# Kernel tuning notes

Measured on AMD Instinct MI355X. Metric: run time of the kernel, lower is better.

Reference implementation:

```python
import jax, jax.numpy as jnp
import numpy as np

N = 100_000; E = 1_600_000; G = 64
D_IN = 128; POS = 16; HID = 32; HEADS = 4; OUT = 10
D0 = D_IN + POS; D1 = HID * HEADS
LRELU = 0.2; BN_EPS = 1e-5; DIV_W = 0.1


def setup_inputs() -> dict:
    key = jax.random.key(0)
    k = jax.random.split(key, 24)
    nrm = lambda ki, shape, s: jax.random.normal(ki, shape, dtype=jnp.float32) * s
    inp = {}
    inp["x"] = nrm(k[0], (N, D_IN), 1.0)
    inp["edge_index"] = jax.random.randint(k[1], (2, E), 0, N, dtype=jnp.int32)
    inp["batch"] = jnp.sort(jax.random.randint(k[2], (N,), 0, G, dtype=jnp.int32))
    inp["pos_w"] = nrm(k[3], (2, POS), 0.5)
    inp["pos_b"] = nrm(k[4], (POS,), 0.1)
    inp["w0"] = nrm(k[5], (D0, HEADS * HID), D0 ** -0.5)
    inp["asrc0"] = nrm(k[6], (HEADS, HID), HID ** -0.5)
    inp["adst0"] = nrm(k[7], (HEADS, HID), HID ** -0.5)
    inp["b0"] = nrm(k[8], (D1,), 0.1)
    inp["w1"] = nrm(k[9], (D1, HEADS * HID), D1 ** -0.5)
    inp["asrc1"] = nrm(k[10], (HEADS, HID), HID ** -0.5)
    inp["adst1"] = nrm(k[11], (HEADS, HID), HID ** -0.5)
    inp["b1"] = nrm(k[12], (D1,), 0.1)
    inp["bn_gamma"] = 1.0 + nrm(k[13], (2, D1), 0.1)
    inp["bn_beta"] = nrm(k[14], (2, D1), 0.1)
    inp["bn_mean"] = nrm(k[15], (2, D1), 0.1)
    inp["bn_var"] = jax.random.uniform(k[16], (2, D1), dtype=jnp.float32, minval=0.5, maxval=1.5)
    inp["proj"] = nrm(k[17], (2, HEADS, HID), HID ** -0.5)
    inp["res_w"] = nrm(k[18], (D1, D1), D1 ** -0.5)
    inp["res_b"] = nrm(k[19], (D1,), 0.1)
    inp["task_w"] = nrm(k[20], (D1, OUT), D1 ** -0.5)
    inp["task_b"] = nrm(k[21], (OUT,), 0.1)
    return inp


def _positions(batch):
    # vectorized version of the per-node Python loop: grid layout per graph
    counts = jnp.bincount(batch, length=G)               # nodes per graph
    starts = jnp.cumsum(counts) - counts                  # exclusive cumsum
    local = jnp.arange(N, dtype=counts.dtype) - starts[batch]
    grid = jnp.ceil(jnp.sqrt(counts.astype(jnp.float32))).astype(counts.dtype)
    g = jnp.maximum(grid[batch], 1)
    denom = jnp.maximum(g - 1, 1).astype(jnp.float32)
    row = (local // g).astype(jnp.float32)
    col = (local % g).astype(jnp.float32)
    return jnp.stack([row / denom, col / denom], axis=-1)  # (N, 2)


def _gat(x, src, dst, w, a_src, a_dst, bias):
    # PyG GATConv (v1) with self-loops already appended to src/dst
    n = x.shape[0]
    h = (x @ w).reshape(n, HEADS, HID)                     # (N, H, C)
    e = jax.nn.leaky_relu(jnp.sum(h * a_src, -1)[src] + jnp.sum(h * a_dst, -1)[dst], LRELU)  # (E+N, H)
    m = jax.lax.stop_gradient(jax.ops.segment_max(e, dst, num_segments=n))
    ex = jnp.exp(e - m[dst])
    alpha = ex / jax.ops.segment_sum(ex, dst, num_segments=n)[dst]
    out = jax.ops.segment_sum(alpha[:, :, None] * h[src], dst, num_segments=n)
    return out.reshape(n, D1) + bias


def _div_loss(x, proj):
    # per-head projection, then mean pairwise cosine similarity between heads
    p = x.reshape(-1, HEADS, HID) * proj                   # (N, H, C)
    pn = p / jnp.maximum(jnp.linalg.norm(p, axis=-1, keepdims=True), 1e-8)
    M = jnp.einsum('nhd,ngd->hg', pn, pn) / pn.shape[0]    # mean_n cos(h_i, h_j)
    iu = jnp.triu_indices(HEADS, k=1)
    return jnp.mean(M[iu] ** 2)


def _bn(x, gamma, beta, mean, var):
    return (x - mean) * gamma * jax.lax.rsqrt(var + BN_EPS) + beta


def reference(x, edge_index, batch, pos_w, pos_b, w0, asrc0, adst0, b0,
              w1, asrc1, adst1, b1, bn_gamma, bn_beta, bn_mean, bn_var,
              proj, res_w, res_b, task_w, task_b):
    loops = jnp.arange(N, dtype=edge_index.dtype)
    src = jnp.concatenate([edge_index[0], loops])
    dst = jnp.concatenate([edge_index[1], loops])
    pos = _positions(batch)
    h = jnp.concatenate([x, pos @ pos_w + pos_b], axis=1)  # (N, D0)
    # layer 0
    h = _gat(h, src, dst, w0, asrc0, adst0, b0)
    div = _div_loss(h, proj[0])
    h = jax.nn.elu(_bn(h, bn_gamma[0], bn_beta[0], bn_mean[0], bn_var[0]))
    # layer 1 (+ residual projection of previous activation)
    prev = h
    h = _gat(h, src, dst, w1, asrc1, adst1, b1)
    div = div + _div_loss(h, proj[1])
    h = jax.nn.elu(_bn(h, bn_gamma[1], bn_beta[1], bn_mean[1], bn_var[1]))
    h = h + prev @ res_w + res_b
    # global mean pool over graphs
    counts = jnp.bincount(batch, length=G).astype(h.dtype)
    emb = jax.ops.segment_sum(h, batch, num_segments=G) / jnp.maximum(counts, 1.0)[:, None]
    task = emb @ task_w + task_b
    return task, DIV_W * div, emb
```

## Files before the change

### kernel.cpp

```cpp
#include <hip/hip_runtime.h>
#include <hip/hip_bf16.h>

#define N_NODES 100000
#define N_EDGES 1600000
#define G_GRAPHS 64
#define D_IN 128
#define POS_DIM 16
#define HID 32
#define HEADS 4
#define OUT_DIM 10
#define D0 144
#define D1 128
#define LRELU_SLOPE 0.2f
#define BN_EPS 1e-5f
#define DIV_W 0.1f

#define BK_SHIFT 9
#define BK_NODES 512
#define NB 196
#define TILE_E 4096
#define NTILES ((N_EDGES + TILE_E - 1) / TILE_E)

#define K0P 160
#define AGG_BLOCKS 2048
#define AGG_WAVES (AGG_BLOCKS * 4)

typedef __attribute__((ext_vector_type(8))) short short8v;
typedef __attribute__((ext_vector_type(4))) float f32x4;

__device__ __forceinline__ unsigned short f2b(float f) {
    unsigned u = __float_as_uint(f);
    unsigned r = (u + 0x7FFFu + ((u >> 16) & 1u)) >> 16;
    return (unsigned short)r;
}
__device__ __forceinline__ float blo(unsigned v) { return __uint_as_float(v << 16); }
__device__ __forceinline__ float bhi(unsigned v) { return __uint_as_float(v & 0xFFFF0000u); }

__global__ void k_hist(const int* __restrict__ batch, int* __restrict__ counts, int n) {
    __shared__ int hist[G_GRAPHS];
    if (threadIdx.x < G_GRAPHS) hist[threadIdx.x] = 0;
    __syncthreads();
    for (int i = blockIdx.x * blockDim.x + threadIdx.x; i < n; i += gridDim.x * blockDim.x)
        atomicAdd(&hist[batch[i]], 1);
    __syncthreads();
    if (threadIdx.x < G_GRAPHS) atomicAdd(&counts[threadIdx.x], hist[threadIdx.x]);
}

__global__ void k_gridstats(const int* __restrict__ counts, int* __restrict__ starts,
                            int* __restrict__ gridg) {
    if (threadIdx.x == 0) {
        int run = 0;
        for (int g = 0; g < G_GRAPHS; ++g) {
            starts[g] = run;
            int c = counts[g];
            run += c;
            int s = (int)sqrtf((float)c);
            while ((long long)s * s < c) ++s;
            while (s > 0 && (long long)(s - 1) * (s - 1) >= c) --s;
            gridg[g] = s;
        }
    }
}

__global__ void k_pos(const int* __restrict__ batch, const int* __restrict__ starts,
                      const int* __restrict__ gridg, float2* __restrict__ pos2) {
    int t = blockIdx.x * blockDim.x + threadIdx.x;
    if (t >= N_NODES) return;
    int b = batch[t];
    int local = t - starts[b];
    int g = max(gridg[b], 1);
    float denom = (float)max(g - 1, 1);
    int r = local / g;
    int c = local - r * g;
    pos2[t] = make_float2((float)r / denom, (float)c / denom);
}

__global__ void k_wprep(const float* __restrict__ w0, const float* __restrict__ w1,
                        const float* __restrict__ wr, unsigned short* __restrict__ t0,
                        unsigned short* __restrict__ t1, unsigned short* __restrict__ tr) {
    int t = blockIdx.x * 256 + threadIdx.x;
    if (t < 128 * K0P) {
        int c = t / K0P, k = t % K0P;
        t0[t] = (k < D0) ? f2b(w0[k * 128 + c]) : (unsigned short)0;
    } else if (t < 128 * K0P + 128 * 128) {
        int i = t - 128 * K0P;
        int c = i / 128, k = i % 128;
        t1[i] = f2b(w1[k * 128 + c]);
    } else if (t < 128 * K0P + 2 * 128 * 128) {
        int i = t - 128 * K0P - 128 * 128;
        int c = i / 128, k = i % 128;
        tr[i] = f2b(wr[k * 128 + c]);
    }
}

__global__ void k_bhist(const int* __restrict__ ei, int* __restrict__ bcount) {
    __shared__ int lh[256];
    int tid = threadIdx.x;
    lh[tid] = 0;
    __syncthreads();
    int e = (blockIdx.x * blockDim.x + tid) * 4;
    if (e < N_EDGES) {
        int4 d4 = *reinterpret_cast<const int4*>(ei + N_EDGES + e);
        atomicAdd(&lh[d4.x >> BK_SHIFT], 1);
        atomicAdd(&lh[d4.y >> BK_SHIFT], 1);
        atomicAdd(&lh[d4.z >> BK_SHIFT], 1);
        atomicAdd(&lh[d4.w >> BK_SHIFT], 1);
    }
    __syncthreads();
    if (tid < NB && lh[tid] > 0) atomicAdd(&bcount[tid], lh[tid]);
}

__global__ void k_bscan(const int* __restrict__ bcount, int* __restrict__ bstart,
                        int* __restrict__ bcursor) {
    if (threadIdx.x == 0) {
        int run = 0;
        for (int i = 0; i < NB; ++i) {
            bstart[i] = run;
            bcursor[i] = run;
            run += bcount[i];
        }
        bstart[NB] = run;
    }
}

__global__ __launch_bounds__(256) void k_bucket(const int* __restrict__ ei,
                                                int* __restrict__ bcursor,
                                                int2* __restrict__ pairs) {
    __shared__ int lh[256];
    __shared__ int lstart[256];
    __shared__ int lcur[256];
    __shared__ int gbase[256];
    __shared__ int2 stage[TILE_E];
    const int tid = threadIdx.x;
    const int tile = blockIdx.x * TILE_E;
    const int cnt = min(TILE_E, N_EDGES - tile);
    lh[tid] = 0;
    __syncthreads();
    int sv[16], dv[16];
#pragma unroll
    for (int u = 0; u < 16; ++u) {
        int i = u * 256 + tid;
        if (i < cnt) {
            sv[u] = ei[tile + i];
            dv[u] = ei[N_EDGES + tile + i];
            atomicAdd(&lh[dv[u] >> BK_SHIFT], 1);
        } else {
            sv[u] = -1; dv[u] = -1;
        }
    }
    __syncthreads();
    int own = lh[tid];
    lstart[tid] = own;
    __syncthreads();
    for (int off = 1; off < 256; off <<= 1) {
        int add = (tid >= off) ? lstart[tid - off] : 0;
        __syncthreads();
        lstart[tid] += add;
        __syncthreads();
    }
    int excl = lstart[tid] - own;
    __syncthreads();
    lstart[tid] = excl;
    lcur[tid] = excl;
    __syncthreads();
#pragma unroll
    for (int u = 0; u < 16; ++u) {
        if (dv[u] >= 0) {
            int b = dv[u] >> BK_SHIFT;
            int slot = atomicAdd(&lcur[b], 1);
            stage[slot] = make_int2(sv[u], dv[u]);
        }
    }
    __syncthreads();
    if (tid < NB && own > 0) gbase[tid] = atomicAdd(&bcursor[tid], own);
    __syncthreads();
    for (int i = tid; i < cnt; i += 256) {
        int2 pr = stage[i];
        int b = pr.y >> BK_SHIFT;
        pairs[gbase[b] + (i - lstart[b])] = pr;
    }
}

__global__ __launch_bounds__(256) void k_csr(const int2* __restrict__ pairs,
                                             const int* __restrict__ bstart,
                                             int* __restrict__ offs,
                                             int* __restrict__ csr_src) {
    __shared__ int ldeg[BK_NODES];
    __shared__ int sm[256];
    __shared__ int lcur[BK_NODES];
    const int b = blockIdx.x;
    const int tid = threadIdx.x;
    const int nb0 = b * BK_NODES;
    const int base = bstart[b];
    const int ecnt = bstart[b + 1] - base;
    ldeg[tid] = 0; ldeg[tid + 256] = 0;
    __syncthreads();
    for (int i = tid; i < ecnt; i += 256)
        atomicAdd(&ldeg[pairs[base + i].y - nb0], 1);
    __syncthreads();
    int v0 = ldeg[tid * 2], v1 = ldeg[tid * 2 + 1];
    int tsum = v0 + v1;
    sm[tid] = tsum;
    __syncthreads();
    for (int off = 1; off < 256; off <<= 1) {
        int add = (tid >= off) ? sm[tid - off] : 0;
        __syncthreads();
        sm[tid] += add;
        __syncthreads();
    }
    int excl = sm[tid] - tsum;
    int o0 = base + excl;
    int o1 = o0 + v0;
    lcur[tid * 2] = o0;
    lcur[tid * 2 + 1] = o1;
    int n0 = nb0 + tid * 2, n1 = n0 + 1;
    if (n0 < N_NODES) offs[n0] = o0;
    if (n1 < N_NODES) offs[n1] = o1;
    if (b == NB - 1 && tid == 0) offs[N_NODES] = bstart[NB];
    __syncthreads();
    for (int i = tid; i < ecnt; i += 256) {
        int2 pr = pairs[base + i];
        int pos = atomicAdd(&lcur[pr.y - nb0], 1);
        csr_src[pos] = pr.x;
    }
}

template <int K, int POS, int RES, int BF16A>
__global__ __launch_bounds__(256) void k_gemm3(
        const float* __restrict__ in, const unsigned short* __restrict__ inb,
        const float2* __restrict__ pos2,
        const float* __restrict__ posw, const float* __restrict__ posb,
        const unsigned short* __restrict__ wbT,
        const float* __restrict__ asrc, const float* __restrict__ adst,
        float* __restrict__ es, float* __restrict__ ed,
        unsigned short* __restrict__ outb,
        const unsigned short* __restrict__ wbT2, const float* __restrict__ bias2,
        unsigned short* __restrict__ outb2, int n) {
    __shared__ unsigned short At[64 * K];
    const int tid = threadIdx.x;
    const int base = blockIdx.x * 64;
    if (BF16A) {
        constexpr int KC8 = K / 8;
        for (int idx = tid; idx < 64 * KC8; idx += 256) {
            int row = idx / KC8, g = idx % KC8;
            int grow = base + row;
            short8v v = (short8v)(short)0;
            if (grow < n) v = *reinterpret_cast<const short8v*>(inb + (size_t)grow * 128 + g * 8);
            unsigned byteoff = (unsigned)((row * K + g * 8) * 2) ^ (unsigned)((row & 7) << 4);
            *reinterpret_cast<short8v*>(reinterpret_cast<char*>(At) + byteoff) = v;
        }
    } else {
        constexpr int KC4 = K / 4;
        for (int idx = tid; idx < 64 * KC4; idx += 256) {
            int row = idx / KC4, c4 = idx % KC4;
            int grow = base + row;
            float4 v = make_float4(0.f, 0.f, 0.f, 0.f);
            if (grow < n) {
                if (!POS || c4 < 32) {
                    v = reinterpret_cast<const float4*>(in)[(size_t)grow * 32 + c4];
                } else if (c4 < 36) {
                    float2 p = pos2[grow];
                    int q = c4 - 32;
                    float4 w0v = reinterpret_cast<const float4*>(posw)[q];
                    float4 w1v = reinterpret_cast<const float4*>(posw + POS_DIM)[q];
                    float4 bv  = reinterpret_cast<const float4*>(posb)[q];
                    v.x = fmaf(p.x, w0v.x, fmaf(p.y, w1v.x, bv.x));
                    v.y = fmaf(p.x, w0v.y, fmaf(p.y, w1v.y, bv.y));
                    v.z = fmaf(p.x, w0v.z, fmaf(p.y, w1v.z, bv.z));
                    v.w = fmaf(p.x, w0v.w, fmaf(p.y, w1v.w, bv.w));
                }
            }
            ushort4 b4;
            b4.x = f2b(v.x); b4.y = f2b(v.y); b4.z = f2b(v.z); b4.w = f2b(v.w);
            unsigned byteoff = (unsigned)((row * K + c4 * 4) * 2) ^ (unsigned)((row & 7) << 4);
            *reinterpret_cast<ushort4*>(reinterpret_cast<char*>(At) + byteoff) = b4;
        }
    }
    __syncthreads();

    const int wv = tid >> 6;
    const int lane = tid & 63;
    const int lrow = lane & 15;
    const int lk8 = lane >> 4;
    f32x4 acc[4][2];
    f32x4 acc2[RES ? 4 : 1][RES ? 2 : 1];
#pragma unroll
    for (int rt = 0; rt < 4; ++rt) {
#pragma unroll
        for (int ct = 0; ct < 2; ++ct) {
            acc[rt][ct] = (f32x4){0.f, 0.f, 0.f, 0.f};
            if (RES) acc2[rt][ct] = (f32x4){0.f, 0.f, 0.f, 0.f};
        }
    }
    const unsigned short* bp0 = wbT + (size_t)(wv * 32 + lrow) * K + lk8 * 8;
    const unsigned short* bp1 = bp0 + 16 * K;
    const unsigned short* cp0 = RES ? (wbT2 + (size_t)(wv * 32 + lrow) * K + lk8 * 8) : nullptr;
    const unsigned short* cp1 = RES ? cp0 + 16 * K : nullptr;

    for (int k0 = 0; k0 < K; k0 += 32) {
        short8v b0 = *reinterpret_cast<const short8v*>(bp0 + k0);
        short8v b1 = *reinterpret_cast<const short8v*>(bp1 + k0);
        short8v a[4];
#pragma unroll
        for (int rt = 0; rt < 4; ++rt) {
            int row = rt * 16 + lrow;
            unsigned byteoff = (unsigned)((row * K + k0 + lk8 * 8) * 2) ^ (unsigned)((row & 7) << 4);
            a[rt] = *reinterpret_cast<const short8v*>(reinterpret_cast<const char*>(At) + byteoff);
        }
#pragma unroll
        for (int rt = 0; rt < 4; ++rt) {
            acc[rt][0] = __builtin_amdgcn_mfma_f32_16x16x32_bf16(a[rt], b0, acc[rt][0], 0, 0, 0);
            acc[rt][1] = __builtin_amdgcn_mfma_f32_16x16x32_bf16(a[rt], b1, acc[rt][1], 0, 0, 0);
        }
        if (RES) {
            short8v c0 = *reinterpret_cast<const short8v*>(cp0 + k0);
            short8v c1 = *reinterpret_cast<const short8v*>(cp1 + k0);
#pragma unroll
            for (int rt = 0; rt < 4; ++rt) {
                acc2[rt][0] = __builtin_amdgcn_mfma_f32_16x16x32_bf16(a[rt], c0, acc2[rt][0], 0, 0, 0);
                acc2[rt][1] = __builtin_amdgcn_mfma_f32_16x16x32_bf16(a[rt], c1, acc2[rt][1], 0, 0, 0);
            }
        }
    }

    float av0 = asrc[wv * 32 + lrow], av1 = asrc[wv * 32 + 16 + lrow];
    float dv0 = adst[wv * 32 + lrow], dv1 = adst[wv * 32 + 16 + lrow];
    float bb0 = 0.f, bb1 = 0.f;
    if (RES) { bb0 = bias2[wv * 32 + lrow]; bb1 = bias2[wv * 32 + 16 + lrow]; }
#pragma unroll
    for (int rt = 0; rt < 4; ++rt) {
#pragma unroll
        for (int r = 0; r < 4; ++r) {
            int row = rt * 16 + lk8 * 4 + r;
            int grow = base + row;
            bool live = (grow < n);
            float v0 = acc[rt][0][r], v1 = acc[rt][1][r];
            if (live) {
                outb[(size_t)grow * 128 + wv * 32 + lrow] = f2b(v0);
                outb[(size_t)grow * 128 + wv * 32 + 16 + lrow] = f2b(v1);
                if (RES) {
                    outb2[(size_t)grow * 128 + wv * 32 + lrow] = f2b(acc2[rt][0][r] + bb0);
                    outb2[(size_t)grow * 128 + wv * 32 + 16 + lrow] = f2b(acc2[rt][1][r] + bb1);
                }
            }
            float ps = v0 * av0 + v1 * av1;
            float pd = v0 * dv0 + v1 * dv1;
            ps += __shfl_xor(ps, 1); pd += __shfl_xor(pd, 1);
            ps += __shfl_xor(ps, 2); pd += __shfl_xor(pd, 2);
            ps += __shfl_xor(ps, 4); pd += __shfl_xor(pd, 4);
            ps += __shfl_xor(ps, 8); pd += __shfl_xor(pd, 8);
            if (lrow == 0 && live) {
                es[grow * 4 + wv] = ps;
                ed[grow * 4 + wv] = pd;
            }
        }
    }
}

template <int LAYER>
__global__ __launch_bounds__(256) void k_aggf(
        const int* __restrict__ csr_src, const int* __restrict__ offs,
        const float* __restrict__ es, const float* __restrict__ ed,
        const unsigned* __restrict__ hb32, const float* __restrict__ bias,
        const float* __restrict__ proj, const float* __restrict__ gamma,
        const float* __restrict__ beta, const float* __restrict__ mean,
        const float* __restrict__ var, float* __restrict__ Msum,
        const unsigned* __restrict__ rbuf16, unsigned* __restrict__ outb16,
        float* __restrict__ outf) {
    __shared__ float smp[6];
    const int tid = threadIdx.x;
    if (tid < 6) smp[tid] = 0.f;
    __syncthreads();
    const int lane = tid & 63;
    const int hd = lane >> 4;
    const int wave_id = blockIdx.x * 4 + (tid >> 6);
    float2 pj = reinterpret_cast<const float2*>(proj)[lane];
    float2 g2 = reinterpret_cast<const float2*>(gamma)[lane];
    float2 b2 = reinterpret_cast<const float2*>(beta)[lane];
    float2 m2 = reinterpret_cast<const float2*>(mean)[lane];
    float2 v2 = reinterpret_cast<const float2*>(var)[lane];
    float scx = g2.x * rsqrtf(v2.x + BN_EPS);
    float scy = g2.y * rsqrtf(v2.y + BN_EPS);
    float bx = bias[lane * 2], by = bias[lane * 2 + 1];
    float accA = 0.f, accB = 0.f, accC = 0.f;

    for (int node = wave_id; node < N_NODES; node += AGG_WAVES) {
        float edv = ed[node * 4 + hd];
        int rs = offs[node], re_ = offs[node + 1];
        float ax[4] = {0.f, 0.f, 0.f, 0.f};
        float ay[4] = {0.f, 0.f, 0.f, 0.f};
        float ds[4] = {0.f, 0.f, 0.f, 0.f};
        int j = rs;
        for (; j + 8 <= re_; j += 8) {
            int s[8];
            float e[8];
            unsigned q[8];
#pragma unroll
            for (int u = 0; u < 8; ++u) s[u] = csr_src[j + u];
#pragma unroll
            for (int u = 0; u < 8; ++u) e[u] = es[s[u] * 4 + hd];
#pragma unroll
            for (int u = 0; u < 8; ++u) q[u] = hb32[(size_t)s[u] * 64 + lane];
#pragma unroll
            for (int u = 0; u < 8; ++u) {
                float a = e[u] + edv;
                a = (a > 0.f) ? a : LRELU_SLOPE * a;
                float x = __expf(a);
                ax[u & 3] = fmaf(x, blo(q[u]), ax[u & 3]);
                ay[u & 3] = fmaf(x, bhi(q[u]), ay[u & 3]);
                ds[u & 3] += x;
            }
        }
        for (; j < re_; ++j) {
            int s = csr_src[j];
            float a = es[s * 4 + hd] + edv;
            a = (a > 0.f) ? a : LRELU_SLOPE * a;
            float x = __expf(a);
            unsigned hv = hb32[(size_t)s * 64 + lane];
            ax[0] = fmaf(x, blo(hv), ax[0]);
            ay[0] = fmaf(x, bhi(hv), ay[0]);
            ds[0] += x;
        }
        {
            float a = es[node * 4 + hd] + edv;
            a = (a > 0.f) ? a : LRELU_SLOPE * a;
            float x = __expf(a);
            unsigned hv = hb32[(size_t)node * 64 + lane];
            ax[0] = fmaf(x, blo(hv), ax[0]);
            ay[0] = fmaf(x, bhi(hv), ay[0]);
            ds[0] += x;
        }
        float inv = 1.f / (ds[0] + ds[1] + ds[2] + ds[3]);
        float ox_ = fmaf(ax[0] + ax[1] + ax[2] + ax[3], inv, bx);
        float oy_ = fmaf(ay[0] + ay[1] + ay[2] + ay[3], inv, by);

        float px = ox_ * pj.x, py = oy_ * pj.y;
        float nn = px * px + py * py;
        nn += __shfl_xor(nn, 1); nn += __shfl_xor(nn, 2);
        nn += __shfl_xor(nn, 4); nn += __shfl_xor(nn, 8);
        float tx = __shfl_xor(px, 16), ty = __shfl_xor(py, 16);
        float d16 = px * tx + py * ty;
        tx = __shfl_xor(px, 32); ty = __shfl_xor(py, 32);
        float d32 = px * tx + py * ty;
        tx = __shfl_xor(px, 48); ty = __shfl_xor(py, 48);
        float d48 = px * tx + py * ty;
        d16 += __shfl_xor(d16, 1); d16 += __shfl_xor(d16, 2);
        d16 += __shfl_xor(d16, 4); d16 += __shfl_xor(d16, 8);
        d32 += __shfl_xor(d32, 1); d32 += __shfl_xor(d32, 2);
        d32 += __shfl_xor(d32, 4); d32 += __shfl_xor(d32, 8);
        d48 += __shfl_xor(d48, 1); d48 += __shfl_xor(d48, 2);
        d48 += __shfl_xor(d48, 4); d48 += __shfl_xor(d48, 8);
        float n_own = fmaxf(sqrtf(nn), 1e-8f);
        float n16 = fmaxf(sqrtf(__shfl_xor(nn, 16)), 1e-8f);
        float n32 = fmaxf(sqrtf(__shfl_xor(nn, 32)), 1e-8f);
        float n48 = fmaxf(sqrtf(__shfl_xor(nn, 48)), 1e-8f);
        accA += d16 / (n_own * n16);
        accB += d32 / (n_own * n32);
        accC += d48 / (n_own * n48);

        float yx = (ox_ - m2.x) * scx + b2.x;
        float yy = (oy_ - m2.y) * scy + b2.y;
        yx = (yx > 0.f) ? yx : (__expf(yx) - 1.f);
        yy = (yy > 0.f) ? yy : (__expf(yy) - 1.f);
        if (LAYER == 1) {
            unsigned rb = rbuf16[(size_t)node * 64 + lane];
            yx += blo(rb);
            yy += bhi(rb);
            reinterpret_cast<float2*>(outf)[(size_t)node * 64 + lane] = make_float2(yx, yy);
        } else {
            outb16[(size_t)node * 64 + lane] = (unsigned)f2b(yx) | ((unsigned)f2b(yy) << 16);
        }
    }

    int g = lane >> 4;
    if ((lane & 15) == 0) {
        if (g == 0) {
            atomicAdd(&smp[0], accA);
            atomicAdd(&smp[1], accB);
            atomicAdd(&smp[2], accC);
        } else if (g == 1) {
            atomicAdd(&smp[4], accB);
            atomicAdd(&smp[3], accC);
        } else if (g == 2) {
            atomicAdd(&smp[5], accA);
        }
    }
    __syncthreads();
    if (tid < 6) unsafeAtomicAdd(&Msum[tid], smp[tid]);
}

__global__ __launch_bounds__(256) void k_pool2(const float* __restrict__ h,
                                               const int* __restrict__ batch,
                                               float* __restrict__ emb) {
    const int tid = threadIdx.x;
    const int lane = tid & 63;
    const int wid = tid >> 6;
    const int wave_id = blockIdx.x * 4 + wid;
    const int CH = (N_NODES + 4095) / 4096;
    const int start = wave_id * CH;
    const int end = min(start + CH, N_NODES);
    float ex = 0.f, ey = 0.f;
    int curg = -1;
    for (int node = start; node < end; ++node) {
        float2 hv = reinterpret_cast<const float2*>(h)[(size_t)node * 64 + lane];
        int g = batch[node];
        if (g != curg) {
            if (curg >= 0) {
                unsafeAtomicAdd(&emb[curg * 128 + lane * 2], ex);
                unsafeAtomicAdd(&emb[curg * 128 + lane * 2 + 1], ey);
            }
            curg = g; ex = 0.f; ey = 0.f;
        }
        ex += hv.x; ey += hv.y;
    }
    if (curg >= 0) {
        unsafeAtomicAdd(&emb[curg * 128 + lane * 2], ex);
        unsafeAtomicAdd(&emb[curg * 128 + lane * 2 + 1], ey);
    }
}

__global__ void k_final(const float* __restrict__ emb_ws, const int* __restrict__ counts,
                        const float* __restrict__ task_w, const float* __restrict__ task_b,
                        const float* __restrict__ Msum, float* __restrict__ out) {
    __shared__ float e_lds[G_GRAPHS * 128];
    __shared__ float cnt[G_GRAPHS];
    int tid = threadIdx.x;
    if (tid < G_GRAPHS) cnt[tid] = fmaxf((float)counts[tid], 1.f);
    __syncthreads();
    for (int i = tid; i < G_GRAPHS * 128; i += 256) {
        float v = emb_ws[i] / cnt[i >> 7];
        e_lds[i] = v;
        out[641 + i] = v;
    }
    __syncthreads();
    for (int p = tid; p < G_GRAPHS * OUT_DIM; p += 256) {
        int g = p / OUT_DIM, o = p % OUT_DIM;
        float acc = task_b[o];
#pragma unroll 8
        for (int k = 0; k < 128; ++k) acc = fmaf(e_lds[g * 128 + k], task_w[k * OUT_DIM + o], acc);
        out[p] = acc;
    }
    if (tid == 0) {
        float div = 0.f;
        for (int l = 0; l < 2; ++l) {
            float s = 0.f;
            for (int p = 0; p < 6; ++p) {
                float m = Msum[l * 6 + p] / (float)N_NODES;
                s = fmaf(m, m, s);
            }
            div += s / 6.f;
        }
        out[G_GRAPHS * OUT_DIM] = DIV_W * div;
    }
}

extern "C" void kernel_launch(void* const* d_in, const int* in_sizes, int n_in,
                              void* d_out, int out_size, void* d_ws, size_t ws_size,
                              hipStream_t stream) {
    const float* x      = (const float*)d_in[0];
    const int*   ei     = (const int*)d_in[1];
    const int*   batch  = (const int*)d_in[2];
    const float* pos_w  = (const float*)d_in[3];
    const float* pos_b  = (const float*)d_in[4];
    const float* w0     = (const float*)d_in[5];
    const float* asrc0  = (const float*)d_in[6];
    const float* adst0  = (const float*)d_in[7];
    const float* b0     = (const float*)d_in[8];
    const float* w1     = (const float*)d_in[9];
    const float* asrc1  = (const float*)d_in[10];
    const float* adst1  = (const float*)d_in[11];
    const float* b1     = (const float*)d_in[12];
    const float* bn_gamma = (const float*)d_in[13];
    const float* bn_beta  = (const float*)d_in[14];
    const float* bn_mean  = (const float*)d_in[15];
    const float* bn_var   = (const float*)d_in[16];
    const float* proj   = (const float*)d_in[17];
    const float* res_w  = (const float*)d_in[18];
    const float* res_b  = (const float*)d_in[19];
    const float* task_w = (const float*)d_in[20];
    const float* task_b = (const float*)d_in[21];
    float* out = (float*)d_out;

    unsigned short* wbT0 = (unsigned short*)d_ws;
    unsigned short* wbT1 = wbT0 + 128 * K0P;
    unsigned short* wbTr = wbT1 + 128 * 128;
    unsigned short* hb   = wbTr + 128 * 128;
    unsigned short* hb0  = hb + (size_t)N_NODES * 128;
    unsigned short* bbuf = hb0 + (size_t)N_NODES * 128;
    float* p = (float*)(bbuf + (size_t)N_NODES * 128);
    float* abuf = p; p += (size_t)N_NODES * D1;
    float* es   = p; p += (size_t)N_NODES * 4;
    float* ed   = p; p += (size_t)N_NODES * 4;
    float2* pos2 = (float2*)p; p += (size_t)N_NODES * 2;
    float* emb  = p; p += G_GRAPHS * 128;
    float* Msum = p; p += 16;
    int* counts = (int*)p;
    int* starts  = counts + G_GRAPHS;
    int* gridg   = starts + G_GRAPHS;
    int* bcount  = gridg + G_GRAPHS;
    int* bstart  = bcount + NB;
    int* bcursor = bstart + NB + 1;
    int* offs    = bcursor + NB;
    int* csr_src = (int*)(((uintptr_t)(offs + N_NODES + 1) + 15) & ~(uintptr_t)15);
    int2* pairs  = (int2*)(csr_src + N_EDGES + 8);

    const int B = 256;

    hipMemsetAsync(counts, 0, G_GRAPHS * sizeof(int), stream);
    hipMemsetAsync(Msum, 0, 12 * sizeof(float), stream);
    hipMemsetAsync(bcount, 0, NB * sizeof(int), stream);
    hipMemsetAsync(emb, 0, G_GRAPHS * 128 * sizeof(float), stream);
    hipMemsetAsync(csr_src + N_EDGES, 0, 8 * sizeof(int), stream);
    k_hist<<<256, B, 0, stream>>>(batch, counts, N_NODES);
    k_gridstats<<<1, 64, 0, stream>>>(counts, starts, gridg);
    k_pos<<<(N_NODES + B - 1) / B, B, 0, stream>>>(batch, starts, gridg, pos2);
    k_wprep<<<(128 * K0P + 2 * 128 * 128 + 255) / 256, 256, 0, stream>>>(
        w0, w1, res_w, wbT0, wbT1, wbTr);

    k_bhist<<<(N_EDGES / 4 + B - 1) / B, B, 0, stream>>>(ei, bcount);
    k_bscan<<<1, 64, 0, stream>>>(bcount, bstart, bcursor);
    k_bucket<<<NTILES, B, 0, stream>>>(ei, bcursor, pairs);
    k_csr<<<NB, B, 0, stream>>>(pairs, bstart, offs, csr_src);

    const int GB = (N_NODES + 63) / 64;

    k_gemm3<K0P, 1, 0, 0><<<GB, 256, 0, stream>>>(
        x, nullptr, pos2, pos_w, pos_b, wbT0, asrc0, adst0, es, ed, hb,
        nullptr, nullptr, nullptr, N_NODES);
    k_aggf<0><<<AGG_BLOCKS, B, 0, stream>>>(
        csr_src, offs, es, ed, (const unsigned*)hb, b0, proj,
        bn_gamma, bn_beta, bn_mean, bn_var, Msum,
        nullptr, (unsigned*)hb0, nullptr);

    k_gemm3<D1, 0, 1, 1><<<GB, 256, 0, stream>>>(
        nullptr, hb0, nullptr, nullptr, nullptr, wbT1, asrc1, adst1, es, ed, hb,
        wbTr, res_b, bbuf, N_NODES);
    k_aggf<1><<<AGG_BLOCKS, B, 0, stream>>>(
        csr_src, offs, es, ed, (const unsigned*)hb, b1, proj + HEADS * HID,
        bn_gamma + D1, bn_beta + D1, bn_mean + D1, bn_var + D1, Msum + 6,
        (const unsigned*)bbuf, nullptr, abuf);

    k_pool2<<<1024, B, 0, stream>>>(abuf, batch, emb);
    k_final<<<1, B, 0, stream>>>(emb, counts, task_w, task_b, Msum, out);
}
```

Before: 527.0 us.

## Split GAT aggregation from diversity/BN epilogue, fuse pooling into layer-1 epilogue

Aggregation now runs as its own kernel with one wave per node and one launch covering all nodes, writing fp32 results to a scratch buffer. The diversity-loss, batch-norm, ELU and residual work moves to a separate streaming kernel that walks contiguous node chunks. For layer 1 that kernel also does the graph mean-pool accumulation, which removes the separate pooling kernel and the write of the final activation. The aim is better load balance and latency hiding in the gather-heavy aggregation. The cost is an extra fp32 round trip of the aggregated features through memory for each layer.

```diff
diff --git a/kernel.cpp b/kernel.cpp
--- a/kernel.cpp
+++ b/kernel.cpp
@@ -22,8 +22,6 @@
 #define NTILES ((N_EDGES + TILE_E - 1) / TILE_E)
 
 #define K0P 160
-#define AGG_BLOCKS 2048
-#define AGG_WAVES (AGG_BLOCKS * 4)
 
 typedef __attribute__((ext_vector_type(8))) short short8v;
 typedef __attribute__((ext_vector_type(4))) float f32x4;
@@ -357,23 +355,84 @@
     }
 }
 
+__global__ void k_aggb(const int* __restrict__ csr_src, const int* __restrict__ offs,
+                       const float* __restrict__ es, const float* __restrict__ ed,
+                       const unsigned* __restrict__ hb32, const float* __restrict__ bias,
+                       float* __restrict__ out) {
+    int node = blockIdx.x * 4 + (threadIdx.x >> 6);
+    if (node >= N_NODES) return;
+    int lane = threadIdx.x & 63;
+    int hd = lane >> 4;
+    float edv = ed[node * 4 + hd];
+    int rs = offs[node], re_ = offs[node + 1];
+    float ax[4] = {0.f, 0.f, 0.f, 0.f};
+    float ay[4] = {0.f, 0.f, 0.f, 0.f};
+    float ds[4] = {0.f, 0.f, 0.f, 0.f};
+    int j = rs;
+    for (; j + 8 <= re_; j += 8) {
+        int s[8];
+        float e[8];
+        unsigned q[8];
+#pragma unroll
+        for (int u = 0; u < 8; ++u) s[u] = csr_src[j + u];
+#pragma unroll
+        for (int u = 0; u < 8; ++u) e[u] = es[s[u] * 4 + hd];
+#pragma unroll
+        for (int u = 0; u < 8; ++u) q[u] = hb32[(size_t)s[u] * 64 + lane];
+#pragma unroll
+        for (int u = 0; u < 8; ++u) {
+            float a = e[u] + edv;
+            a = (a > 0.f) ? a : LRELU_SLOPE * a;
+            float x = __expf(a);
+            ax[u & 3] = fmaf(x, blo(q[u]), ax[u & 3]);
+            ay[u & 3] = fmaf(x, bhi(q[u]), ay[u & 3]);
+            ds[u & 3] += x;
+        }
+    }
+    for (; j < re_; ++j) {
+        int s = csr_src[j];
+        float a = es[s * 4 + hd] + edv;
+        a = (a > 0.f) ? a : LRELU_SLOPE * a;
+        float x = __expf(a);
+        unsigned hv = hb32[(size_t)s * 64 + lane];
+        ax[0] = fmaf(x, blo(hv), ax[0]);
+        ay[0] = fmaf(x, bhi(hv), ay[0]);
+        ds[0] += x;
+    }
+    {
+        float a = es[node * 4 + hd] + edv;
+        a = (a > 0.f) ? a : LRELU_SLOPE * a;
+        float x = __expf(a);
+        unsigned hv = hb32[(size_t)node * 64 + lane];
+        ax[0] = fmaf(x, blo(hv), ax[0]);
+        ay[0] = fmaf(x, bhi(hv), ay[0]);
+        ds[0] += x;
+    }
+    float inv = 1.f / (ds[0] + ds[1] + ds[2] + ds[3]);
+    float2 o;
+    o.x = fmaf(ax[0] + ax[1] + ax[2] + ax[3], inv, bias[lane * 2]);
+    o.y = fmaf(ay[0] + ay[1] + ay[2] + ay[3], inv, bias[lane * 2 + 1]);
+    reinterpret_cast<float2*>(out)[(size_t)node * 64 + lane] = o;
+}
+
 template <int LAYER>
-__global__ __launch_bounds__(256) void k_aggf(
-        const int* __restrict__ csr_src, const int* __restrict__ offs,
-        const float* __restrict__ es, const float* __restrict__ ed,
-        const unsigned* __restrict__ hb32, const float* __restrict__ bias,
+__global__ __launch_bounds__(256) void k_divbn(
+        const float* __restrict__ hin, const unsigned* __restrict__ rbuf16,
         const float* __restrict__ proj, const float* __restrict__ gamma,
         const float* __restrict__ beta, const float* __restrict__ mean,
         const float* __restrict__ var, float* __restrict__ Msum,
-        const unsigned* __restrict__ rbuf16, unsigned* __restrict__ outb16,
-        float* __restrict__ outf) {
-    __shared__ float smp[6];
+        unsigned* __restrict__ outb16,
+        const int* __restrict__ batch, float* __restrict__ emb) {
+    __shared__ float sm[6];
     const int tid = threadIdx.x;
-    if (tid < 6) smp[tid] = 0.f;
+    if (tid < 6) sm[tid] = 0.f;
     __syncthreads();
     const int lane = tid & 63;
-    const int hd = lane >> 4;
-    const int wave_id = blockIdx.x * 4 + (tid >> 6);
+    const int wid = tid >> 6;
+    const int wave_id = blockIdx.x * 4 + wid;
+    const int CH = (N_NODES + 4095) / 4096;
+    const int start = wave_id * CH;
+    const int end = min(start + CH, N_NODES);
     float2 pj = reinterpret_cast<const float2*>(proj)[lane];
     float2 g2 = reinterpret_cast<const float2*>(gamma)[lane];
     float2 b2 = reinterpret_cast<const float2*>(beta)[lane];
@@ -381,60 +440,12 @@
     float2 v2 = reinterpret_cast<const float2*>(var)[lane];
     float scx = g2.x * rsqrtf(v2.x + BN_EPS);
     float scy = g2.y * rsqrtf(v2.y + BN_EPS);
-    float bx = bias[lane * 2], by = bias[lane * 2 + 1];
     float accA = 0.f, accB = 0.f, accC = 0.f;
-
-    for (int node = wave_id; node < N_NODES; node += AGG_WAVES) {
-        float edv = ed[node * 4 + hd];
-        int rs = offs[node], re_ = offs[node + 1];
-        float ax[4] = {0.f, 0.f, 0.f, 0.f};
-        float ay[4] = {0.f, 0.f, 0.f, 0.f};
-        float ds[4] = {0.f, 0.f, 0.f, 0.f};
-        int j = rs;
-        for (; j + 8 <= re_; j += 8) {
-            int s[8];
-            float e[8];
-            unsigned q[8];
-#pragma unroll
-            for (int u = 0; u < 8; ++u) s[u] = csr_src[j + u];
-#pragma unroll
-            for (int u = 0; u < 8; ++u) e[u] = es[s[u] * 4 + hd];
-#pragma unroll
-            for (int u = 0; u < 8; ++u) q[u] = hb32[(size_t)s[u] * 64 + lane];
-#pragma unroll
-            for (int u = 0; u < 8; ++u) {
-                float a = e[u] + edv;
-                a = (a > 0.f) ? a : LRELU_SLOPE * a;
-                float x = __expf(a);
-                ax[u & 3] = fmaf(x, blo(q[u]), ax[u & 3]);
-                ay[u & 3] = fmaf(x, bhi(q[u]), ay[u & 3]);
-                ds[u & 3] += x;
-            }
-        }
-        for (; j < re_; ++j) {
-            int s = csr_src[j];
-            float a = es[s * 4 + hd] + edv;
-            a = (a > 0.f) ? a : LRELU_SLOPE * a;
-            float x = __expf(a);
-            unsigned hv = hb32[(size_t)s * 64 + lane];
-            ax[0] = fmaf(x, blo(hv), ax[0]);
-            ay[0] = fmaf(x, bhi(hv), ay[0]);
-            ds[0] += x;
-        }
-        {
-            float a = es[node * 4 + hd] + edv;
-            a = (a > 0.f) ? a : LRELU_SLOPE * a;
-            float x = __expf(a);
-            unsigned hv = hb32[(size_t)node * 64 + lane];
-            ax[0] = fmaf(x, blo(hv), ax[0]);
-            ay[0] = fmaf(x, bhi(hv), ay[0]);
-            ds[0] += x;
-        }
-        float inv = 1.f / (ds[0] + ds[1] + ds[2] + ds[3]);
-        float ox_ = fmaf(ax[0] + ax[1] + ax[2] + ax[3], inv, bx);
-        float oy_ = fmaf(ay[0] + ay[1] + ay[2] + ay[3], inv, by);
-
-        float px = ox_ * pj.x, py = oy_ * pj.y;
+    float ex = 0.f, ey = 0.f;
+    int curg = -1;
+    for (int node = start; node < end; ++node) {
+        float2 hv = reinterpret_cast<const float2*>(hin)[(size_t)node * 64 + lane];
+        float px = hv.x * pj.x, py = hv.y * pj.y;
         float nn = px * px + py * py;
         nn += __shfl_xor(nn, 1); nn += __shfl_xor(nn, 2);
         nn += __shfl_xor(nn, 4); nn += __shfl_xor(nn, 8);
@@ -457,66 +468,46 @@
         accA += d16 / (n_own * n16);
         accB += d32 / (n_own * n32);
         accC += d48 / (n_own * n48);
-
-        float yx = (ox_ - m2.x) * scx + b2.x;
-        float yy = (oy_ - m2.y) * scy + b2.y;
+        float yx = (hv.x - m2.x) * scx + b2.x;
+        float yy = (hv.y - m2.y) * scy + b2.y;
         yx = (yx > 0.f) ? yx : (__expf(yx) - 1.f);
         yy = (yy > 0.f) ? yy : (__expf(yy) - 1.f);
         if (LAYER == 1) {
             unsigned rb = rbuf16[(size_t)node * 64 + lane];
             yx += blo(rb);
             yy += bhi(rb);
-            reinterpret_cast<float2*>(outf)[(size_t)node * 64 + lane] = make_float2(yx, yy);
+            int g = batch[node];
+            if (g != curg) {
+                if (curg >= 0) {
+                    unsafeAtomicAdd(&emb[curg * 128 + lane * 2], ex);
+                    unsafeAtomicAdd(&emb[curg * 128 + lane * 2 + 1], ey);
+                }
+                curg = g; ex = 0.f; ey = 0.f;
+            }
+            ex += yx; ey += yy;
         } else {
             outb16[(size_t)node * 64 + lane] = (unsigned)f2b(yx) | ((unsigned)f2b(yy) << 16);
         }
     }
-
+    if (LAYER == 1 && curg >= 0) {
+        unsafeAtomicAdd(&emb[curg * 128 + lane * 2], ex);
+        unsafeAtomicAdd(&emb[curg * 128 + lane * 2 + 1], ey);
+    }
     int g = lane >> 4;
     if ((lane & 15) == 0) {
         if (g == 0) {
-            atomicAdd(&smp[0], accA);
-            atomicAdd(&smp[1], accB);
-            atomicAdd(&smp[2], accC);
+            atomicAdd(&sm[0], accA);
+            atomicAdd(&sm[1], accB);
+            atomicAdd(&sm[2], accC);
         } else if (g == 1) {
-            atomicAdd(&smp[4], accB);
-            atomicAdd(&smp[3], accC);
+            atomicAdd(&sm[4], accB);
+            atomicAdd(&sm[3], accC);
         } else if (g == 2) {
-            atomicAdd(&smp[5], accA);
-        }
-    }
-    __syncthreads();
-    if (tid < 6) unsafeAtomicAdd(&Msum[tid], smp[tid]);
-}
-
-__global__ __launch_bounds__(256) void k_pool2(const float* __restrict__ h,
-                                               const int* __restrict__ batch,
-                                               float* __restrict__ emb) {
-    const int tid = threadIdx.x;
-    const int lane = tid & 63;
-    const int wid = tid >> 6;
-    const int wave_id = blockIdx.x * 4 + wid;
-    const int CH = (N_NODES + 4095) / 4096;
-    const int start = wave_id * CH;
-    const int end = min(start + CH, N_NODES);
-    float ex = 0.f, ey = 0.f;
-    int curg = -1;
-    for (int node = start; node < end; ++node) {
-        float2 hv = reinterpret_cast<const float2*>(h)[(size_t)node * 64 + lane];
-        int g = batch[node];
-        if (g != curg) {
-            if (curg >= 0) {
-                unsafeAtomicAdd(&emb[curg * 128 + lane * 2], ex);
-                unsafeAtomicAdd(&emb[curg * 128 + lane * 2 + 1], ey);
-            }
-            curg = g; ex = 0.f; ey = 0.f;
-        }
-        ex += hv.x; ey += hv.y;
-    }
-    if (curg >= 0) {
-        unsafeAtomicAdd(&emb[curg * 128 + lane * 2], ex);
-        unsafeAtomicAdd(&emb[curg * 128 + lane * 2 + 1], ey);
-    }
+            atomicAdd(&sm[5], accA);
+        }
+    }
+    __syncthreads();
+    if (tid < 6) unsafeAtomicAdd(&Msum[tid], sm[tid]);
 }
 
 __global__ void k_final(const float* __restrict__ emb_ws, const int* __restrict__ counts,
@@ -623,23 +614,23 @@
     k_csr<<<NB, B, 0, stream>>>(pairs, bstart, offs, csr_src);
 
     const int GB = (N_NODES + 63) / 64;
+    const int AB = (N_NODES + 3) / 4;
 
     k_gemm3<K0P, 1, 0, 0><<<GB, 256, 0, stream>>>(
         x, nullptr, pos2, pos_w, pos_b, wbT0, asrc0, adst0, es, ed, hb,
         nullptr, nullptr, nullptr, N_NODES);
-    k_aggf<0><<<AGG_BLOCKS, B, 0, stream>>>(
-        csr_src, offs, es, ed, (const unsigned*)hb, b0, proj,
-        bn_gamma, bn_beta, bn_mean, bn_var, Msum,
-        nullptr, (unsigned*)hb0, nullptr);
+    k_aggb<<<AB, B, 0, stream>>>(csr_src, offs, es, ed, (const unsigned*)hb, b0, abuf);
+    k_divbn<0><<<1024, B, 0, stream>>>(
+        abuf, nullptr, proj, bn_gamma, bn_beta, bn_mean, bn_var, Msum,
+        (unsigned*)hb0, nullptr, nullptr);
 
     k_gemm3<D1, 0, 1, 1><<<GB, 256, 0, stream>>>(
         nullptr, hb0, nullptr, nullptr, nullptr, wbT1, asrc1, adst1, es, ed, hb,
         wbTr, res_b, bbuf, N_NODES);
-    k_aggf<1><<<AGG_BLOCKS, B, 0, stream>>>(
-        csr_src, offs, es, ed, (const unsigned*)hb, b1, proj + HEADS * HID,
-        bn_gamma + D1, bn_beta + D1, bn_mean + D1, bn_var + D1, Msum + 6,
-        (const unsigned*)bbuf, nullptr, abuf);
-
-    k_pool2<<<1024, B, 0, stream>>>(abuf, batch, emb);
+    k_aggb<<<AB, B, 0, stream>>>(csr_src, offs, es, ed, (const unsigned*)hb, b1, abuf);
+    k_divbn<1><<<1024, B, 0, stream>>>(
+        abuf, (const unsigned*)bbuf, proj + HEADS * HID, bn_gamma + D1, bn_beta + D1,
+        bn_mean + D1, bn_var + D1, Msum + 6, nullptr, batch, emb);
+
     k_final<<<1, B, 0, stream>>>(emb, counts, task_w, task_b, Msum, out);
 }
```

Result: faster. 497.8 us (-5.6%).
